# Kernel tuning notes

Measured on AMD Instinct MI355X. Metric: run time of the kernel, lower is better.

Reference implementation:

```python
import jax, jax.numpy as jnp
import numpy as np

B, C, O = 16384, 128, 128


def setup_inputs() -> dict:
    key = jax.random.key(0)
    k1, k2, k3 = jax.random.split(key, 3)
    x = jax.random.normal(k1, (B, C, 3, 3), dtype=jnp.float32)
    # 9 stacked Conv2d(C, O, 3x3) weights/biases, position p = 3*r + c (row-major)
    W = jax.random.normal(k2, (9, O, C, 3, 3), dtype=jnp.float32) * 0.05
    b = jax.random.normal(k3, (9, O), dtype=jnp.float32) * 0.05
    return {"x": x, "W": W, "b": b}


def reference(x, W, b):
    Bn = x.shape[0]
    xr = x.reshape(Bn, C, 3, 3)
    # F.interpolate(scale_factor=3, mode='nearest'): each pixel replicated 3x3
    ins = jnp.repeat(jnp.repeat(xr, 3, axis=2), 3, axis=3)  # (B, C, 9, 9)
    # patch for output position (r, c) is ins[:, :, 2+r:5+r, 2+c:5+c]
    patches = jnp.stack(
        [ins[:, :, 2 + r:5 + r, 2 + c:5 + c] for r in range(3) for c in range(3)],
        axis=0,
    )  # (9, B, C, 3, 3)
    # each conv reduces its 3x3xC patch to one pixel per out-channel
    out = jnp.einsum('pbcij,pocij->bpo', patches, W) + b[None]  # (B, 9, O)
    out = out.transpose(0, 2, 1).reshape(Bn, O, 3, 3)  # row-major (r, c)
    return out
```

## Files before the change

kernel.cpp:

```cpp
#include <hip/hip_runtime.h>
#include <hip/hip_bf16.h>

typedef __bf16 bf16_t;
typedef __attribute__((ext_vector_type(8))) __bf16 bf16x8;
typedef __attribute__((ext_vector_type(4))) float f32x4;

#define KDIM 1152
#define NDIM 1152
#define BM 128
#define BN 192
#define BK 32
#define NIT 36
#define NTILES 6
#define A_STEP 8192
#define A_PANEL 294912
#define B_STEP 12288
#define B_TILE (36 * B_STEP)
#define CVT_BLOCKS 9216

__device__ __forceinline__ void gload_lds16(const void* g, void* l) {
    __builtin_amdgcn_global_load_lds(
        (const __attribute__((address_space(1))) void*)g,
        (__attribute__((address_space(3))) void*)l, 16, 0, 0);
}

__global__ void prep(const float* __restrict__ X, bf16_t* __restrict__ Xb,
                     const float* __restrict__ W, const float* __restrict__ bvec,
                     bf16_t* __restrict__ Bm, float* __restrict__ bias)
{
    __shared__ char L[4096];
    const int bid = blockIdx.x;
    const int tid = threadIdx.x;
    if (bid < CVT_BLOCKS) {
        const int wv = (bid << 2) + (tid >> 6);
        const int l = tid & 63;
        const int P = wv / 288;
        const int rem = wv - P * 288;
        const int T = rem >> 3;
        const int rb = rem & 7;
        const int row = P * 128 + rb * 16 + (l >> 2);
        const int k = T * 32 + (l & 3) * 8;
        const float* src = X + (size_t)row * KDIM + k;
        f32x4 lo = *(const f32x4*)src;
        f32x4 hi = *(const f32x4*)(src + 4);
        bf16x8 v;
        #pragma unroll
        for (int e = 0; e < 4; ++e) { v[e] = (__bf16)lo[e]; v[4 + e] = (__bf16)hi[e]; }
        char* wl = L + (tid >> 6) * 1024;
        *(bf16x8*)(wl + ((l & 3) * 16 + (l >> 2)) * 16) = v;
        __builtin_amdgcn_s_barrier();
        bf16x8 o = *(const bf16x8*)(wl + l * 16);
        *(bf16x8*)((char*)Xb + ((size_t)wv * 64 + l) * 16) = o;
        return;
    }
    const int t = (bid - CVT_BLOCKS) * 256 + tid;
    if (t < NDIM) {
        const int o = t / 9, p = t - o * 9;
        bias[t] = bvec[p * 128 + o];
    }
    const int c = t & 127;
    const int o = (t >> 7) & 127;
    const int p = t >> 14;
    if (p >= 9) return;
    const int r = p / 3, cc = p - r * 3;
    float eff[3][3] = {{0.f,0.f,0.f},{0.f,0.f,0.f},{0.f,0.f,0.f}};
    const float* w = W + (size_t)((p * 128 + o) * 128 + c) * 9;
    #pragma unroll
    for (int i = 0; i < 3; ++i) {
        const int a = (2 + r + i) / 3;
        #pragma unroll
        for (int j = 0; j < 3; ++j) {
            const int bb = (2 + cc + j) / 3;
            eff[a][bb] += w[i * 3 + j];
        }
    }
    const int n = o * 9 + p;
    const int tile = n / BN;
    const int nin = n - tile * BN;
    #pragma unroll
    for (int a = 0; a < 3; ++a)
        #pragma unroll
        for (int bb = 0; bb < 3; ++bb) {
            const int k = c * 9 + a * 3 + bb;
            const size_t idx = (size_t)tile * (B_TILE / 2)
                             + (k >> 5) * (B_STEP / 2)
                             + (nin >> 4) * 512 + ((k >> 3) & 3) * 128
                             + (nin & 15) * 8 + (k & 7);
            Bm[idx] = (bf16_t)eff[a][bb];
        }
}

__launch_bounds__(256, 3)
__global__ void ind_gemm(const bf16_t* __restrict__ Xb,
                         const bf16_t* __restrict__ Bm,
                         const float* __restrict__ bias,
                         float* __restrict__ out)
{
    __shared__ char Bs[2][B_STEP];

    const int tid = threadIdx.x;
    const int lane = tid & 63;
    const int wid = tid >> 6;
    const int wm = wid >> 1;
    const int wn = wid & 1;

    const int bid = blockIdx.x;
    const int swz = (bid & 7) * 96 + (bid >> 3);
    const int mt = swz / NTILES;
    const int nt = swz - mt * NTILES;
    const int m0 = mt * BM;

    const int fr = (lane >> 4) * 256 + (lane & 15) * 16;
    const char* apl = (const char*)Xb + (size_t)mt * A_PANEL + wm * 4096 + fr;
    const char* bpanel = (const char*)Bm + (size_t)nt * B_TILE;

    f32x4 acc[4][6];
    #pragma unroll
    for (int i = 0; i < 4; ++i)
        #pragma unroll
        for (int j = 0; j < 6; ++j)
            acc[i][j] = (f32x4){0.f, 0.f, 0.f, 0.f};

    f32x4 afA[4], afB[4];
    bf16x8 bfr[6];

    #define LOADA(T, AF) do {                                               \
        const char* p_ = apl + (size_t)(T) * A_STEP;                        \
        asm volatile("global_load_dwordx4 %0, %4, off\n\t"                  \
                     "global_load_dwordx4 %1, %4, off offset:1024\n\t"      \
                     "global_load_dwordx4 %2, %4, off offset:2048\n\t"      \
                     "global_load_dwordx4 %3, %4, off offset:3072"          \
                     : "=&v"(AF[0]), "=&v"(AF[1]), "=&v"(AF[2]), "=&v"(AF[3]) \
                     : "v"(p_) : "memory");                                 \
    } while (0)

    #define GLDB(T, BUF) do {                                               \
        const char* s_ = bpanel + (size_t)(T) * B_STEP;                     \
        _Pragma("unroll")                                                   \
        for (int r_ = 0; r_ < 3; ++r_) {                                    \
            const int u_ = (tid + r_ * 256) * 16;                           \
            gload_lds16(s_ + u_, &Bs[BUF][u_]);                             \
        } } while (0)

    #define RDB(CUR) do {                                                   \
        _Pragma("unroll")                                                   \
        for (int j_ = 0; j_ < 6; ++j_)                                      \
            bfr[j_] = *(const bf16x8*)(&Bs[CUR][(wn * 6 + j_) * 1024 + fr]); \
        asm volatile("s_waitcnt lgkmcnt(0)" ::: "memory");                  \
        __builtin_amdgcn_sched_barrier(0);                                  \
        __builtin_amdgcn_s_barrier();                                       \
    } while (0)

    #define MFMA24(AF) do {                                                 \
        __builtin_amdgcn_s_setprio(1);                                      \
        _Pragma("unroll")                                                   \
        for (int mi = 0; mi < 4; ++mi) {                                    \
            const bf16x8 a_ = __builtin_bit_cast(bf16x8, AF[mi]);           \
            _Pragma("unroll")                                               \
            for (int j_ = 0; j_ < 6; ++j_)                                  \
                acc[mi][j_] = __builtin_amdgcn_mfma_f32_16x16x32_bf16(      \
                    a_, bfr[j_], acc[mi][j_], 0, 0, 0);                     \
        }                                                                   \
        __builtin_amdgcn_s_setprio(0);                                      \
    } while (0)

    #define WAITV(N) do {                                                   \
        asm volatile("s_waitcnt vmcnt(" #N ")" ::: "memory");               \
        __builtin_amdgcn_sched_barrier(0);                                  \
    } while (0)

    LOADA(0, afA);
    GLDB(0, 0);
    LOADA(1, afB);
    GLDB(1, 1);
    WAITV(7);
    __builtin_amdgcn_s_barrier();

    #pragma unroll 1
    for (int t2 = 0; t2 < 17; ++t2) {
        const int t = 2 * t2;
        RDB(0);
        GLDB(t + 2, 0);
        MFMA24(afA);
        LOADA(t + 2, afA);
        WAITV(7);
        __builtin_amdgcn_s_barrier();
        RDB(1);
        GLDB(t + 3, 1);
        MFMA24(afB);
        LOADA(t + 3, afB);
        WAITV(7);
        __builtin_amdgcn_s_barrier();
    }
    RDB(0);
    MFMA24(afA);
    WAITV(0);
    __builtin_amdgcn_s_barrier();
    RDB(1);
    MFMA24(afB);

    #undef LOADA
    #undef GLDB
    #undef RDB
    #undef MFMA24
    #undef WAITV

    const int orow = (lane >> 4) * 4;
    const int ocol = lane & 15;
    const int gn0 = nt * BN + wn * 96 + ocol;
    #pragma unroll
    for (int ni = 0; ni < 6; ++ni) {
        const float bv = bias[gn0 + ni * 16];
        #pragma unroll
        for (int mi = 0; mi < 4; ++mi) {
            float* po = out + (size_t)(m0 + wm * 64 + mi * 16 + orow) * NDIM
                            + gn0 + ni * 16;
            #pragma unroll
            for (int r = 0; r < 4; ++r)
                po[(size_t)r * NDIM] = acc[mi][ni][r] + bv;
        }
    }
}

extern "C" void kernel_launch(void* const* d_in, const int* in_sizes, int n_in,
                              void* d_out, int out_size, void* d_ws, size_t ws_size,
                              hipStream_t stream)
{
    const float* x  = (const float*)d_in[0];
    const float* W  = (const float*)d_in[1];
    const float* bv = (const float*)d_in[2];
    float* out = (float*)d_out;

    bf16_t* Xb   = (bf16_t*)d_ws;
    bf16_t* Bm   = (bf16_t*)((char*)d_ws + (size_t)16384 * KDIM * sizeof(bf16_t));
    float*  bias = (float*)((char*)Bm + (size_t)KDIM * NDIM * sizeof(bf16_t));

    prep<<<CVT_BLOCKS + 576, 256, 0, stream>>>(x, Xb, W, bv, Bm, bias);
    ind_gemm<<<768, 256, 0, stream>>>(Xb, Bm, bias, out);
}
```

Baseline: 80.77 us.

## Widen GEMM N-tile to 288 and stage A tiles through LDS

Raises the block tile from 128x192 to 128x288, giving 4 N tiles and 512 blocks instead of 6 and 768, so each A panel is re-read fewer times. A tiles are now loaded asynchronously into LDS alongside B instead of directly into registers, and lanes with no B data issue a dummy load into a scrap buffer so every thread keeps the same vmcnt. The bigger tile needs 36 accumulators per thread and more LDS, so occupancy drops from 3 to 2 blocks per SIMD group. The wait count of 7 is left as it was even though each thread now issues 7 loads per stage.

```diff
diff --git a/kernel.cpp b/kernel.cpp
--- a/kernel.cpp
+++ b/kernel.cpp
@@ -8,13 +8,13 @@
 #define KDIM 1152
 #define NDIM 1152
 #define BM 128
-#define BN 192
+#define BN 288
 #define BK 32
 #define NIT 36
-#define NTILES 6
+#define NTILES 4
 #define A_STEP 8192
 #define A_PANEL 294912
-#define B_STEP 12288
+#define B_STEP 18432
 #define B_TILE (36 * B_STEP)
 #define CVT_BLOCKS 9216
 
@@ -90,13 +90,15 @@
         }
 }
 
-__launch_bounds__(256, 3)
+__launch_bounds__(256, 2)
 __global__ void ind_gemm(const bf16_t* __restrict__ Xb,
                          const bf16_t* __restrict__ Bm,
                          const float* __restrict__ bias,
                          float* __restrict__ out)
 {
+    __shared__ char As[2][A_STEP];
     __shared__ char Bs[2][B_STEP];
+    __shared__ char Scrap[1024];
 
     const int tid = threadIdx.x;
     const int lane = tid & 63;
@@ -105,62 +107,59 @@
     const int wn = wid & 1;
 
     const int bid = blockIdx.x;
-    const int swz = (bid & 7) * 96 + (bid >> 3);
-    const int mt = swz / NTILES;
-    const int nt = swz - mt * NTILES;
+    const int swz = (bid & 7) * 64 + (bid >> 3);
+    const int mt = swz >> 2;
+    const int nt = swz & 3;
     const int m0 = mt * BM;
 
     const int fr = (lane >> 4) * 256 + (lane & 15) * 16;
-    const char* apl = (const char*)Xb + (size_t)mt * A_PANEL + wm * 4096 + fr;
+    const char* apanel = (const char*)Xb + (size_t)mt * A_PANEL;
     const char* bpanel = (const char*)Bm + (size_t)nt * B_TILE;
 
-    f32x4 acc[4][6];
+    f32x4 acc[4][9];
     #pragma unroll
     for (int i = 0; i < 4; ++i)
         #pragma unroll
-        for (int j = 0; j < 6; ++j)
+        for (int j = 0; j < 9; ++j)
             acc[i][j] = (f32x4){0.f, 0.f, 0.f, 0.f};
 
-    f32x4 afA[4], afB[4];
-    bf16x8 bfr[6];
-
-    #define LOADA(T, AF) do {                                               \
-        const char* p_ = apl + (size_t)(T) * A_STEP;                        \
-        asm volatile("global_load_dwordx4 %0, %4, off\n\t"                  \
-                     "global_load_dwordx4 %1, %4, off offset:1024\n\t"      \
-                     "global_load_dwordx4 %2, %4, off offset:2048\n\t"      \
-                     "global_load_dwordx4 %3, %4, off offset:3072"          \
-                     : "=&v"(AF[0]), "=&v"(AF[1]), "=&v"(AF[2]), "=&v"(AF[3]) \
-                     : "v"(p_) : "memory");                                 \
-    } while (0)
-
-    #define GLDB(T, BUF) do {                                               \
-        const char* s_ = bpanel + (size_t)(T) * B_STEP;                     \
-        _Pragma("unroll")                                                   \
-        for (int r_ = 0; r_ < 3; ++r_) {                                    \
+    bf16x8 af[4], bfr[9];
+
+    #define GLD(T, BUF) do {                                                \
+        const char* sa_ = apanel + (size_t)(T) * A_STEP;                    \
+        gload_lds16(sa_ + tid * 16,        &As[BUF][tid * 16]);             \
+        gload_lds16(sa_ + 4096 + tid * 16, &As[BUF][4096 + tid * 16]);      \
+        const char* sb_ = bpanel + (size_t)(T) * B_STEP;                    \
+        _Pragma("unroll")                                                   \
+        for (int r_ = 0; r_ < 4; ++r_) {                                    \
             const int u_ = (tid + r_ * 256) * 16;                           \
-            gload_lds16(s_ + u_, &Bs[BUF][u_]);                             \
-        } } while (0)
-
-    #define RDB(CUR) do {                                                   \
-        _Pragma("unroll")                                                   \
-        for (int j_ = 0; j_ < 6; ++j_)                                      \
-            bfr[j_] = *(const bf16x8*)(&Bs[CUR][(wn * 6 + j_) * 1024 + fr]); \
+            gload_lds16(sb_ + u_, &Bs[BUF][u_]);                            \
+        }                                                                   \
+        if (tid < 128) gload_lds16(sb_ + (1024 + tid) * 16,                 \
+                                   &Bs[BUF][(1024 + tid) * 16]);            \
+        else           gload_lds16(bpanel + tid * 16, Scrap);               \
+    } while (0)
+
+    #define RD(CUR) do {                                                    \
+        _Pragma("unroll")                                                   \
+        for (int mi_ = 0; mi_ < 4; ++mi_)                                   \
+            af[mi_] = *(const bf16x8*)(&As[CUR][(wm * 4 + mi_) * 1024 + fr]); \
+        _Pragma("unroll")                                                   \
+        for (int j_ = 0; j_ < 9; ++j_)                                      \
+            bfr[j_] = *(const bf16x8*)(&Bs[CUR][(wn * 9 + j_) * 1024 + fr]); \
         asm volatile("s_waitcnt lgkmcnt(0)" ::: "memory");                  \
         __builtin_amdgcn_sched_barrier(0);                                  \
         __builtin_amdgcn_s_barrier();                                       \
     } while (0)
 
-    #define MFMA24(AF) do {                                                 \
+    #define MFMA36() do {                                                   \
         __builtin_amdgcn_s_setprio(1);                                      \
         _Pragma("unroll")                                                   \
-        for (int mi = 0; mi < 4; ++mi) {                                    \
-            const bf16x8 a_ = __builtin_bit_cast(bf16x8, AF[mi]);           \
+        for (int mi_ = 0; mi_ < 4; ++mi_)                                   \
             _Pragma("unroll")                                               \
-            for (int j_ = 0; j_ < 6; ++j_)                                  \
-                acc[mi][j_] = __builtin_amdgcn_mfma_f32_16x16x32_bf16(      \
-                    a_, bfr[j_], acc[mi][j_], 0, 0, 0);                     \
-        }                                                                   \
+            for (int j_ = 0; j_ < 9; ++j_)                                  \
+                acc[mi_][j_] = __builtin_amdgcn_mfma_f32_16x16x32_bf16(     \
+                    af[mi_], bfr[j_], acc[mi_][j_], 0, 0, 0);               \
         __builtin_amdgcn_s_setprio(0);                                      \
     } while (0)
 
@@ -169,47 +168,42 @@
         __builtin_amdgcn_sched_barrier(0);                                  \
     } while (0)
 
-    LOADA(0, afA);
-    GLDB(0, 0);
-    LOADA(1, afB);
-    GLDB(1, 1);
+    GLD(0, 0);
+    GLD(1, 1);
     WAITV(7);
     __builtin_amdgcn_s_barrier();
 
     #pragma unroll 1
     for (int t2 = 0; t2 < 17; ++t2) {
         const int t = 2 * t2;
-        RDB(0);
-        GLDB(t + 2, 0);
-        MFMA24(afA);
-        LOADA(t + 2, afA);
+        RD(0);
+        GLD(t + 2, 0);
+        MFMA36();
         WAITV(7);
         __builtin_amdgcn_s_barrier();
-        RDB(1);
-        GLDB(t + 3, 1);
-        MFMA24(afB);
-        LOADA(t + 3, afB);
+        RD(1);
+        GLD(t + 3, 1);
+        MFMA36();
         WAITV(7);
         __builtin_amdgcn_s_barrier();
     }
-    RDB(0);
-    MFMA24(afA);
+    RD(0);
+    MFMA36();
     WAITV(0);
     __builtin_amdgcn_s_barrier();
-    RDB(1);
-    MFMA24(afB);
-
-    #undef LOADA
-    #undef GLDB
-    #undef RDB
-    #undef MFMA24
+    RD(1);
+    MFMA36();
+
+    #undef GLD
+    #undef RD
+    #undef MFMA36
     #undef WAITV
 
     const int orow = (lane >> 4) * 4;
     const int ocol = lane & 15;
-    const int gn0 = nt * BN + wn * 96 + ocol;
-    #pragma unroll
-    for (int ni = 0; ni < 6; ++ni) {
+    const int gn0 = nt * BN + wn * 144 + ocol;
+    #pragma unroll
+    for (int ni = 0; ni < 9; ++ni) {
         const float bv = bias[gn0 + ni * 16];
         #pragma unroll
         for (int mi = 0; mi < 4; ++mi) {
@@ -236,5 +230,5 @@
     float*  bias = (float*)((char*)Bm + (size_t)KDIM * NDIM * sizeof(bf16_t));
 
     prep<<<CVT_BLOCKS + 576, 256, 0, stream>>>(x, Xb, W, bv, Bm, bias);
-    ind_gemm<<<768, 256, 0, stream>>>(Xb, Bm, bias, out);
-}
+    ind_gemm<<<512, 256, 0, stream>>>(Xb, Bm, bias, out);
+}
```

After: 79.98 us. No clear change (-1.0%).
